# Kernel tuning notes

Measured on AMD Instinct MI355X. Metric: run time of the kernel, lower is better.

The kernel has to match this reference:

```python
import jax, jax.numpy as jnp
import numpy as np

K1 = 3
K2 = 3


def _lap(adj):
    # faithful to torch lap(): zero diagonal, D0^-1/2 A D1^-1/2 with inf->0
    n = adj.shape[-1]
    adj = adj * (1.0 - jnp.eye(n, dtype=adj.dtype))
    d0 = adj.sum(0) ** -0.5  # column sums, scales rows (as in the torch code)
    d1 = adj.sum(1) ** -0.5  # row sums, scales cols
    d0 = jnp.where(jnp.isinf(d0), 0.0, d0)
    d1 = jnp.where(jnp.isinf(d1), 0.0, d1)
    return d0[:, None] * adj * d1[None, :]


def setup_inputs() -> dict:
    key = jax.random.key(0)
    kx, ka, kw, kb = jax.random.split(key, 4)
    B, N, C, OUT = 8, 200, 32, 64
    fan_in = C * K1 * K2  # 288
    bound = 1.0 / np.sqrt(fan_in)
    x = jax.random.normal(kx, (B, N, N, C), dtype=jnp.float32)
    adj = jax.random.uniform(ka, (N, N), dtype=jnp.float32)
    weight = jax.random.uniform(kw, (OUT, fan_in), dtype=jnp.float32, minval=-bound, maxval=bound)
    bias = jax.random.uniform(kb, (OUT,), dtype=jnp.float32, minval=-bound, maxval=bound)
    return {"x": x, "adj": adj, "weight": weight, "bias": bias}


def reference(x, adj, weight, bias):
    L = _lap(adj)

    def left(T):   # contract node axis 1 with L[b, e]
        return jnp.einsum('abcd,be->aecd', T, L)

    def right(T):  # contract node axis 2 with L[e, c]
        return jnp.einsum('abcd,ec->abed', T, L)

    # Chebyshev recursion along left node dim
    lefts = [x]
    if K1 > 1:
        lefts.append(left(x))
    for _ in range(2, K1):
        lefts.append(2.0 * left(lefts[-1]) - lefts[-2])

    # for each left order, Chebyshev recursion along right node dim
    feats = []
    for T in lefts:
        rights = [T]
        if K2 > 1:
            rights.append(right(T))
        for _ in range(2, K2):
            rights.append(2.0 * right(rights[-1]) - rights[-2])
        feats.extend(rights)  # k1-major, k2-minor order

    B, N = x.shape[0], x.shape[1]
    Tx = jnp.stack(feats, axis=3)              # [B, N, N, K1*K2, C]
    Tx2 = Tx.reshape(B, N, N, -1)              # flatten (K1, K2, C) -> matches torch permute+reshape
    return Tx2 @ weight.T + bias               # [B, N, N, out]
```

## Files before the change

### kernel.cpp

```cpp
#include <hip/hip_runtime.h>

#define NN 200

typedef short s8v __attribute__((ext_vector_type(8)));
typedef float f4v __attribute__((ext_vector_type(4)));

__device__ __forceinline__ unsigned short f2bf(float f) {
    unsigned u = __float_as_uint(f);
    u += 0x7fffu + ((u >> 16) & 1u);
    return (unsigned short)(u >> 16);
}

__global__ __launch_bounds__(256) void k_sums(const float* __restrict__ adj,
                                              float* __restrict__ cs, float* __restrict__ rs) {
    int t = blockIdx.x;
    int tid = threadIdx.x;
    float c = 0.f, r = 0.f;
    for (int p = tid; p < NN; p += 256) {
        if (p != t) {
            c += adj[p * NN + t];
            r += adj[t * NN + p];
        }
    }
    #pragma unroll
    for (int off = 32; off; off >>= 1) {
        c += __shfl_down(c, off);
        r += __shfl_down(r, off);
    }
    __shared__ float sc[4], sr[4];
    if ((tid & 63) == 0) { sc[tid >> 6] = c; sr[tid >> 6] = r; }
    __syncthreads();
    if (tid == 0) {
        cs[t] = sc[0] + sc[1] + sc[2] + sc[3];
        rs[t] = sr[0] + sr[1] + sr[2] + sr[3];
    }
}

__global__ __launch_bounds__(256) void k_lap2(const float* __restrict__ adj,
    const float* __restrict__ cs, const float* __restrict__ rs,
    float* __restrict__ L, unsigned short* __restrict__ Lh, unsigned short* __restrict__ LTh) {
    int idx = blockIdx.x * 256 + threadIdx.x;
    int p = idx >> 8, q = idx & 255;
    if (p >= 224) return;
    float v = 0.f;
    if (p < NN && q < NN) {
        float a = (p == q) ? 0.f : adj[p * NN + q];
        float d0 = (cs[p] > 0.f) ? rsqrtf(cs[p]) : 0.f;
        float d1 = (rs[q] > 0.f) ? rsqrtf(rs[q]) : 0.f;
        v = d0 * a * d1;
        L[p * NN + q] = v;
    }
    unsigned short h = f2bf(v);
    if (q < 224) Lh[p * 224 + q] = h;
    LTh[q * 224 + p] = h;
}

__global__ __launch_bounds__(256) void k_sq2(const float* __restrict__ L,
    unsigned short* __restrict__ C2h, unsigned short* __restrict__ C2Th) {
    int idx = blockIdx.x * 256 + threadIdx.x;
    int p = idx >> 8, q = idx & 255;
    if (p >= 224) return;
    float v = 0.f;
    if (p < NN && q < NN) {
        float s = 0.f;
        for (int r2 = 0; r2 < NN; ++r2) s += L[p * NN + r2] * L[r2 * NN + q];
        v = 2.f * s - ((p == q) ? 1.f : 0.f);
    }
    unsigned short h = f2bf(v);
    if (q < 224) C2h[p * 224 + q] = h;
    C2Th[q * 224 + p] = h;
}

__global__ __launch_bounds__(256) void k_wprep2(const float* __restrict__ w,
    unsigned short* __restrict__ WmT) {
    int idx = blockIdx.x * 256 + threadIdx.x;
    if (idx < 192 * 96) {
        int n = idx / 96, k = idx - n * 96;
        int k1 = k >> 5, c = k & 31;
        int k2 = n >> 6, o = n & 63;
        WmT[idx] = f2bf(w[o * 288 + (k1 * 3 + k2) * 32 + c]);
    }
}

__global__ __launch_bounds__(256) void k_cast(const float* __restrict__ x,
    unsigned short* __restrict__ Xh, unsigned short* __restrict__ XhT, int a0) {
    int a = blockIdx.z;
    int b0 = blockIdx.y * 32;
    int jc0 = blockIdx.x * 64;
    int tid = threadIdx.x;
    __shared__ unsigned short Xs[32][65];
    const float* xb = x + (size_t)(a0 + a) * (NN * 6400);
    int r = tid >> 6, q = tid & 63;
    #pragma unroll
    for (int k = 0; k < 8; ++k) {
        int rr = r + k * 4;
        int b = b0 + rr;
        float v = (b < NN) ? xb[(size_t)b * 6400 + jc0 + q] : 0.f;
        unsigned short h = f2bf(v);
        Xs[rr][q] = h;
        if (b < NN) Xh[((size_t)a * NN + b) * 6400 + jc0 + q] = h;
    }
    __syncthreads();
    int jcl = tid >> 2, bs = (tid & 3) * 8;
    s8v v;
    #pragma unroll
    for (int j2 = 0; j2 < 8; ++j2) v[j2] = (short)Xs[bs + j2][jcl];
    *(s8v*)(XhT + (size_t)a * (6400 * 224) + (size_t)(jc0 + jcl) * 224 + b0 + bs) = v;
}

__global__ __launch_bounds__(256) void k_y(
    const unsigned short* __restrict__ LTh, const unsigned short* __restrict__ C2Th,
    const unsigned short* __restrict__ XhT,
    unsigned short* __restrict__ Y1, unsigned short* __restrict__ Y2, int i0, int Gi) {
    int a = blockIdx.z;
    int itile = blockIdx.y;
    int jc0 = blockIdx.x << 8;
    int tid = threadIdx.x;
    int w = tid >> 6, l15 = tid & 15, g = (tid & 63) >> 4;

    __shared__ unsigned short As[2][32][40];
    __shared__ unsigned short Xt[256][40];

    const unsigned short* xtb = XhT + (size_t)a * (6400 * 224) + (size_t)jc0 * 224;
    int ibase = i0 + itile * 32;

    f4v z = {0.f, 0.f, 0.f, 0.f};
    f4v acc[2][2][4];
    #pragma unroll
    for (int m = 0; m < 2; ++m)
        #pragma unroll
        for (int f = 0; f < 2; ++f)
            #pragma unroll
            for (int n = 0; n < 4; ++n) acc[m][f][n] = z;

    int amat = tid >> 7, arr = (tid >> 2) & 31, ah = tid & 3;
    const unsigned short* asrc = (amat ? C2Th : LTh) + (size_t)(ibase + arr) * 224 + ah * 8;

    for (int ks = 0; ks < 7; ++ks) {
        int b0 = ks * 32;
        __syncthreads();
        *(s8v*)&As[amat][arr][ah * 8] = *(const s8v*)(asrc + b0);
        const unsigned short* xs = xtb + (size_t)tid * 224 + b0;
        #pragma unroll
        for (int h = 0; h < 4; ++h)
            *(s8v*)&Xt[tid][h * 8] = *(const s8v*)(xs + h * 8);
        __syncthreads();

        s8v bfr[4];
        #pragma unroll
        for (int nf = 0; nf < 4; ++nf)
            bfr[nf] = *(s8v*)&Xt[w * 64 + nf * 16 + l15][g * 8];
        #pragma unroll
        for (int m = 0; m < 2; ++m) {
            #pragma unroll
            for (int f = 0; f < 2; ++f) {
                s8v af = *(s8v*)&As[m][f * 16 + l15][g * 8];
                #pragma unroll
                for (int nf = 0; nf < 4; ++nf)
                    acc[m][f][nf] = __builtin_amdgcn_mfma_f32_16x16x32_bf16(
                        af, bfr[nf], acc[m][f][nf], 0, 0, 0);
            }
        }
    }

    #pragma unroll
    for (int f = 0; f < 2; ++f) {
        #pragma unroll
        for (int r = 0; r < 4; ++r) {
            int il_ = itile * 32 + f * 16 + 4 * g + r;
            if (il_ < Gi && i0 + il_ < NN) {
                size_t base = ((size_t)a * Gi + il_) * 6400 + jc0 + w * 64 + l15;
                #pragma unroll
                for (int nf = 0; nf < 4; ++nf) {
                    Y1[base + nf * 16] = f2bf(acc[0][f][nf][r]);
                    Y2[base + nf * 16] = f2bf(acc[1][f][nf][r]);
                }
            }
        }
    }
}

__global__ __launch_bounds__(256) void k_fused(
    const unsigned short* __restrict__ Xh, const unsigned short* __restrict__ Y1,
    const unsigned short* __restrict__ Y2, const unsigned short* __restrict__ WmT,
    const unsigned short* __restrict__ Lh, const unsigned short* __restrict__ C2h,
    const float* __restrict__ bias, float* __restrict__ out,
    int a0, int i0, int Gi) {
    int tl = blockIdx.x;
    int al = tl / Gi, il = tl - al * Gi;
    int tid = threadIdx.x;
    int w = tid >> 6, l15 = tid & 15, g = (tid & 63) >> 4;

    __shared__ unsigned short EL[2][28][64][8];

    const unsigned short* xrow = Xh + (size_t)(al * NN + i0 + il) * 6400;
    const unsigned short* y1r = Y1 + (size_t)tl * 6400;
    const unsigned short* y2r = Y2 + (size_t)tl * 6400;

    f4v z = {0.f, 0.f, 0.f, 0.f};
    f4v accD[2][2][4];
    #pragma unroll
    for (int jh = 0; jh < 2; ++jh)
        #pragma unroll
        for (int f = 0; f < 2; ++f)
            #pragma unroll
            for (int n = 0; n < 4; ++n) accD[jh][f][n] = z;

    #pragma unroll
    for (int jh = 0; jh < 2; ++jh) {
        int jrow0 = jh * 128 + w * 32;
        s8v afr[3][2];
        #pragma unroll
        for (int f = 0; f < 2; ++f) {
            int j = jrow0 + f * 16 + l15;
            int jc = j < NN ? j : NN - 1;
            afr[0][f] = *(const s8v*)(xrow + jc * 32 + g * 8);
            afr[1][f] = *(const s8v*)(y1r + jc * 32 + g * 8);
            afr[2][f] = *(const s8v*)(y2r + jc * 32 + g * 8);
        }

        f4v accE[2][8];
        #pragma unroll
        for (int f = 0; f < 2; ++f)
            #pragma unroll
            for (int n = 0; n < 8; ++n) accE[f][n] = z;

        #pragma unroll
        for (int s = 0; s < 3; ++s) {
            #pragma unroll
            for (int nf = 0; nf < 12; ++nf) {
                s8v bf = *(const s8v*)(WmT + (nf * 16 + l15) * 96 + s * 32 + g * 8);
                #pragma unroll
                for (int f = 0; f < 2; ++f) {
                    if (nf < 4)
                        accD[jh][f][nf] = __builtin_amdgcn_mfma_f32_16x16x32_bf16(
                            afr[s][f], bf, accD[jh][f][nf], 0, 0, 0);
                    else
                        accE[f][nf - 4] = __builtin_amdgcn_mfma_f32_16x16x32_bf16(
                            afr[s][f], bf, accE[f][nf - 4], 0, 0, 0);
                }
            }
        }

        if (!(jh == 1 && w == 3)) {
            #pragma unroll
            for (int f = 0; f < 2; ++f) {
                int ebase = jrow0 + f * 16;
                #pragma unroll
                for (int nf = 0; nf < 8; ++nf) {
                    int tns = nf >> 2;
                    int o = (nf & 3) * 16 + l15;
                    #pragma unroll
                    for (int r0 = 0; r0 < 4; r0 += 2) {
                        int e = ebase + 4 * g + r0;
                        unsigned short u0 = (e < NN) ? f2bf(accE[f][nf][r0]) : (unsigned short)0;
                        unsigned short u1 = (e + 1 < NN) ? f2bf(accE[f][nf][r0 + 1]) : (unsigned short)0;
                        unsigned pk = (unsigned)u0 | ((unsigned)u1 << 16);
                        *(unsigned*)&EL[tns][e >> 3][o][e & 7] = pk;
                    }
                }
            }
        }
    }

    __syncthreads();

    #pragma unroll
    for (int ks = 0; ks < 7; ++ks) {
        s8v b1[4], b2[4];
        #pragma unroll
        for (int nf = 0; nf < 4; ++nf) {
            b1[nf] = *(const s8v*)&EL[0][4 * ks + g][nf * 16 + l15][0];
            b2[nf] = *(const s8v*)&EL[1][4 * ks + g][nf * 16 + l15][0];
        }
        #pragma unroll
        for (int jh = 0; jh < 2; ++jh) {
            #pragma unroll
            for (int r2 = 0; r2 < 2; ++r2) {
                int jb = jh * 128 + w * 32 + r2 * 16;
                if (jb < NN) {
                    int aoff = (jb + l15) * 224 + ks * 32 + g * 8;
                    s8v a1 = *(const s8v*)(Lh + aoff);
                    s8v a2 = *(const s8v*)(C2h + aoff);
                    #pragma unroll
                    for (int nf = 0; nf < 4; ++nf) {
                        accD[jh][r2][nf] = __builtin_amdgcn_mfma_f32_16x16x32_bf16(
                            a1, b1[nf], accD[jh][r2][nf], 0, 0, 0);
                        accD[jh][r2][nf] = __builtin_amdgcn_mfma_f32_16x16x32_bf16(
                            a2, b2[nf], accD[jh][r2][nf], 0, 0, 0);
                    }
                }
            }
        }
    }

    float bv[4];
    #pragma unroll
    for (int nf = 0; nf < 4; ++nf) bv[nf] = bias[nf * 16 + l15];
    float* ob = out + ((size_t)(a0 + al) * NN + (i0 + il)) * 12800;
    #pragma unroll
    for (int jh = 0; jh < 2; ++jh) {
        #pragma unroll
        for (int r2 = 0; r2 < 2; ++r2) {
            int jb = jh * 128 + w * 32 + r2 * 16;
            if (jb < NN) {
                #pragma unroll
                for (int r = 0; r < 4; ++r) {
                    int j = jb + 4 * g + r;
                    if (j < NN) {
                        #pragma unroll
                        for (int nf = 0; nf < 4; ++nf)
                            ob[(size_t)j * 64 + nf * 16 + l15] = accD[jh][r2][nf][r] + bv[nf];
                    }
                }
            }
        }
    }
}

extern "C" void kernel_launch(void* const* d_in, const int* in_sizes, int n_in,
                              void* d_out, int out_size, void* d_ws, size_t ws_size,
                              hipStream_t stream) {
    const float* x    = (const float*)d_in[0];
    const float* adj  = (const float*)d_in[1];
    const float* w    = (const float*)d_in[2];
    const float* bias = (const float*)d_in[3];
    float* out = (float*)d_out;

    char* ws = (char*)d_ws;
    size_t off = 0;
    auto alloc = [&](size_t bytes) { size_t p = off; off = (off + bytes + 255) & ~(size_t)255; return p; };
    float* cs = (float*)(ws + alloc(NN * 4));
    float* rs = (float*)(ws + alloc(NN * 4));
    float* L  = (float*)(ws + alloc(NN * NN * 4));
    unsigned short* Lh   = (unsigned short*)(ws + alloc(224 * 224 * 2));
    unsigned short* C2h  = (unsigned short*)(ws + alloc(224 * 224 * 2));
    unsigned short* LTh  = (unsigned short*)(ws + alloc(256 * 224 * 2));
    unsigned short* C2Th = (unsigned short*)(ws + alloc(256 * 224 * 2));
    unsigned short* WmT  = (unsigned short*)(ws + alloc(192 * 96 * 2));
    size_t fixedEnd = off;

    const int cfgA[8] = {8, 8, 8, 8, 4, 2, 1, 1};
    const int cfgG[8] = {200, 100, 50, 25, 25, 25, 25, 5};
    size_t perA = (size_t)NN * 6400 * 2 + (size_t)6400 * 224 * 2;
    size_t perR = (size_t)2 * 6400 * 2;
    int Ab = 1, Gi = 5;
    for (int k = 0; k < 8; ++k) {
        size_t R_ = (size_t)cfgA[k] * cfgG[k];
        size_t need = fixedEnd + (size_t)cfgA[k] * perA + R_ * perR + 8192;
        if (need <= ws_size) { Ab = cfgA[k]; Gi = cfgG[k]; break; }
    }
    int R = Ab * Gi;
    unsigned short* Xh  = (unsigned short*)(ws + alloc((size_t)Ab * NN * 6400 * 2));
    unsigned short* XhT = (unsigned short*)(ws + alloc((size_t)Ab * 6400 * 224 * 2));
    unsigned short* Y1  = (unsigned short*)(ws + alloc((size_t)R * 6400 * 2));
    unsigned short* Y2  = (unsigned short*)(ws + alloc((size_t)R * 6400 * 2));

    k_sums<<<dim3(NN), dim3(256), 0, stream>>>(adj, cs, rs);
    k_lap2<<<dim3(224), dim3(256), 0, stream>>>(adj, cs, rs, L, Lh, LTh);
    k_sq2<<<dim3(224), dim3(256), 0, stream>>>(L, C2h, C2Th);
    k_wprep2<<<dim3(72), dim3(256), 0, stream>>>(w, WmT);

    int nIT = (Gi + 31) / 32;
    for (int a0 = 0; a0 < 8; a0 += Ab) {
        k_cast<<<dim3(100, 7, Ab), dim3(256), 0, stream>>>(x, Xh, XhT, a0);
        for (int i0 = 0; i0 < NN; i0 += Gi) {
            k_y<<<dim3(25, nIT, Ab), dim3(256), 0, stream>>>(LTh, C2Th, XhT, Y1, Y2, i0, Gi);
            k_fused<<<dim3(R), dim3(256), 0, stream>>>(Xh, Y1, Y2, WmT, Lh, C2h, bias, out, a0, i0, Gi);
        }
    }
}
```

Before: 310.1 us.

## Split fused kernel work across eight waves instead of four with two halves

```diff
diff --git a/kernel.cpp b/kernel.cpp
--- a/kernel.cpp
+++ b/kernel.cpp
@@ -180,7 +180,7 @@
     }
 }
 
-__global__ __launch_bounds__(256) void k_fused(
+__global__ __launch_bounds__(512, 4) void k_fused(
     const unsigned short* __restrict__ Xh, const unsigned short* __restrict__ Y1,
     const unsigned short* __restrict__ Y2, const unsigned short* __restrict__ WmT,
     const unsigned short* __restrict__ Lh, const unsigned short* __restrict__ C2h,
@@ -189,7 +189,7 @@
     int tl = blockIdx.x;
     int al = tl / Gi, il = tl - al * Gi;
     int tid = threadIdx.x;
-    int w = tid >> 6, l15 = tid & 15, g = (tid & 63) >> 4;
+    int wv = tid >> 6, l15 = tid & 15, g = (tid & 63) >> 4;
 
     __shared__ unsigned short EL[2][28][64][8];
 
@@ -198,72 +198,59 @@
     const unsigned short* y2r = Y2 + (size_t)tl * 6400;
 
     f4v z = {0.f, 0.f, 0.f, 0.f};
-    f4v accD[2][2][4];
-    #pragma unroll
-    for (int jh = 0; jh < 2; ++jh)
-        #pragma unroll
-        for (int f = 0; f < 2; ++f)
-            #pragma unroll
-            for (int n = 0; n < 4; ++n) accD[jh][f][n] = z;
-
-    #pragma unroll
-    for (int jh = 0; jh < 2; ++jh) {
-        int jrow0 = jh * 128 + w * 32;
-        s8v afr[3][2];
+    f4v accD[2][4];
+    #pragma unroll
+    for (int f = 0; f < 2; ++f)
+        #pragma unroll
+        for (int n = 0; n < 4; ++n) accD[f][n] = z;
+
+    if (wv < 7) {
         #pragma unroll
         for (int f = 0; f < 2; ++f) {
-            int j = jrow0 + f * 16 + l15;
-            int jc = j < NN ? j : NN - 1;
-            afr[0][f] = *(const s8v*)(xrow + jc * 32 + g * 8);
-            afr[1][f] = *(const s8v*)(y1r + jc * 32 + g * 8);
-            afr[2][f] = *(const s8v*)(y2r + jc * 32 + g * 8);
-        }
-
-        f4v accE[2][8];
-        #pragma unroll
-        for (int f = 0; f < 2; ++f)
-            #pragma unroll
-            for (int n = 0; n < 8; ++n) accE[f][n] = z;
-
-        #pragma unroll
-        for (int s = 0; s < 3; ++s) {
-            #pragma unroll
-            for (int nf = 0; nf < 12; ++nf) {
-                s8v bf = *(const s8v*)(WmT + (nf * 16 + l15) * 96 + s * 32 + g * 8);
-                #pragma unroll
-                for (int f = 0; f < 2; ++f) {
+            int jrow = wv * 32 + f * 16 + l15;
+            int jc = jrow < NN ? jrow : NN - 1;
+            s8v afr[3];
+            afr[0] = *(const s8v*)(xrow + jc * 32 + g * 8);
+            afr[1] = *(const s8v*)(y1r + jc * 32 + g * 8);
+            afr[2] = *(const s8v*)(y2r + jc * 32 + g * 8);
+
+            f4v accE[8];
+            #pragma unroll
+            for (int n = 0; n < 8; ++n) accE[n] = z;
+
+            #pragma unroll
+            for (int s = 0; s < 3; ++s) {
+                #pragma unroll
+                for (int nf = 0; nf < 12; ++nf) {
+                    s8v bf = *(const s8v*)(WmT + (nf * 16 + l15) * 96 + s * 32 + g * 8);
                     if (nf < 4)
-                        accD[jh][f][nf] = __builtin_amdgcn_mfma_f32_16x16x32_bf16(
-                            afr[s][f], bf, accD[jh][f][nf], 0, 0, 0);
+                        accD[f][nf] = __builtin_amdgcn_mfma_f32_16x16x32_bf16(
+                            afr[s], bf, accD[f][nf], 0, 0, 0);
                     else
-                        accE[f][nf - 4] = __builtin_amdgcn_mfma_f32_16x16x32_bf16(
-                            afr[s][f], bf, accE[f][nf - 4], 0, 0, 0);
-                }
-            }
-        }
-
-        if (!(jh == 1 && w == 3)) {
-            #pragma unroll
-            for (int f = 0; f < 2; ++f) {
-                int ebase = jrow0 + f * 16;
-                #pragma unroll
-                for (int nf = 0; nf < 8; ++nf) {
-                    int tns = nf >> 2;
-                    int o = (nf & 3) * 16 + l15;
-                    #pragma unroll
-                    for (int r0 = 0; r0 < 4; r0 += 2) {
-                        int e = ebase + 4 * g + r0;
-                        unsigned short u0 = (e < NN) ? f2bf(accE[f][nf][r0]) : (unsigned short)0;
-                        unsigned short u1 = (e + 1 < NN) ? f2bf(accE[f][nf][r0 + 1]) : (unsigned short)0;
-                        unsigned pk = (unsigned)u0 | ((unsigned)u1 << 16);
-                        *(unsigned*)&EL[tns][e >> 3][o][e & 7] = pk;
-                    }
+                        accE[nf - 4] = __builtin_amdgcn_mfma_f32_16x16x32_bf16(
+                            afr[s], bf, accE[nf - 4], 0, 0, 0);
+                }
+            }
+
+            int ebase = wv * 32 + f * 16;
+            #pragma unroll
+            for (int nf = 0; nf < 8; ++nf) {
+                int tns = nf >> 2;
+                int o = (nf & 3) * 16 + l15;
+                #pragma unroll
+                for (int r0 = 0; r0 < 4; r0 += 2) {
+                    int e = ebase + 4 * g + r0;
+                    unsigned short u0 = (e < NN) ? f2bf(accE[nf][r0]) : (unsigned short)0;
+                    unsigned short u1 = (e + 1 < NN) ? f2bf(accE[nf][r0 + 1]) : (unsigned short)0;
+                    unsigned pk = (unsigned)u0 | ((unsigned)u1 << 16);
+                    *(unsigned*)&EL[tns][e >> 3][o][e & 7] = pk;
                 }
             }
         }
     }
 
     __syncthreads();
+    if (wv == 7) return;
 
     #pragma unroll
     for (int ks = 0; ks < 7; ++ks) {
@@ -274,21 +261,18 @@
             b2[nf] = *(const s8v*)&EL[1][4 * ks + g][nf * 16 + l15][0];
         }
         #pragma unroll
-        for (int jh = 0; jh < 2; ++jh) {
-            #pragma unroll
-            for (int r2 = 0; r2 < 2; ++r2) {
-                int jb = jh * 128 + w * 32 + r2 * 16;
-                if (jb < NN) {
-                    int aoff = (jb + l15) * 224 + ks * 32 + g * 8;
-                    s8v a1 = *(const s8v*)(Lh + aoff);
-                    s8v a2 = *(const s8v*)(C2h + aoff);
-                    #pragma unroll
-                    for (int nf = 0; nf < 4; ++nf) {
-                        accD[jh][r2][nf] = __builtin_amdgcn_mfma_f32_16x16x32_bf16(
-                            a1, b1[nf], accD[jh][r2][nf], 0, 0, 0);
-                        accD[jh][r2][nf] = __builtin_amdgcn_mfma_f32_16x16x32_bf16(
-                            a2, b2[nf], accD[jh][r2][nf], 0, 0, 0);
-                    }
+        for (int r2 = 0; r2 < 2; ++r2) {
+            int jb = wv * 32 + r2 * 16;
+            if (jb < NN) {
+                int aoff = (jb + l15) * 224 + ks * 32 + g * 8;
+                s8v a1 = *(const s8v*)(Lh + aoff);
+                s8v a2 = *(const s8v*)(C2h + aoff);
+                #pragma unroll
+                for (int nf = 0; nf < 4; ++nf) {
+                    accD[r2][nf] = __builtin_amdgcn_mfma_f32_16x16x32_bf16(
+                        a1, b1[nf], accD[r2][nf], 0, 0, 0);
+                    accD[r2][nf] = __builtin_amdgcn_mfma_f32_16x16x32_bf16(
+                        a2, b2[nf], accD[r2][nf], 0, 0, 0);
                 }
             }
         }
@@ -299,19 +283,16 @@
     for (int nf = 0; nf < 4; ++nf) bv[nf] = bias[nf * 16 + l15];
     float* ob = out + ((size_t)(a0 + al) * NN + (i0 + il)) * 12800;
     #pragma unroll
-    for (int jh = 0; jh < 2; ++jh) {
-        #pragma unroll
-        for (int r2 = 0; r2 < 2; ++r2) {
-            int jb = jh * 128 + w * 32 + r2 * 16;
-            if (jb < NN) {
-                #pragma unroll
-                for (int r = 0; r < 4; ++r) {
-                    int j = jb + 4 * g + r;
-                    if (j < NN) {
-                        #pragma unroll
-                        for (int nf = 0; nf < 4; ++nf)
-                            ob[(size_t)j * 64 + nf * 16 + l15] = accD[jh][r2][nf][r] + bv[nf];
-                    }
+    for (int r2 = 0; r2 < 2; ++r2) {
+        int jb = wv * 32 + r2 * 16;
+        if (jb < NN) {
+            #pragma unroll
+            for (int r = 0; r < 4; ++r) {
+                int j = jb + 4 * g + r;
+                if (j < NN) {
+                    #pragma unroll
+                    for (int nf = 0; nf < 4; ++nf)
+                        ob[(size_t)j * 64 + nf * 16 + l15] = accD[r2][nf][r] + bv[nf];
                 }
             }
         }
@@ -366,7 +347,7 @@
         k_cast<<<dim3(100, 7, Ab), dim3(256), 0, stream>>>(x, Xh, XhT, a0);
         for (int i0 = 0; i0 < NN; i0 += Gi) {
             k_y<<<dim3(25, nIT, Ab), dim3(256), 0, stream>>>(LTh, C2Th, XhT, Y1, Y2, i0, Gi);
-            k_fused<<<dim3(R), dim3(256), 0, stream>>>(Xh, Y1, Y2, WmT, Lh, C2h, bias, out, a0, i0, Gi);
-        }
-    }
-}
+            k_fused<<<dim3(R), dim3(512), 0, stream>>>(Xh, Y1, Y2, WmT, Lh, C2h, bias, out, a0, i0, Gi);
+        }
+    }
+}
```

New measurement: 341.0 us. 10.0% more time.
